# Kernel optimization log

Measured on AMD Instinct MI355X. Metric: run time of the kernel, lower is better.

Reference implementation:

```python
import jax, jax.numpy as jnp
import numpy as np

B, H, S, DK = 4, 16, 2048, 64


def setup_inputs() -> dict:
    key = jax.random.key(0)
    kq, kk, kv, km = jax.random.split(key, 4)
    Q = jax.random.normal(kq, (B, H, S, DK), dtype=jnp.float32)
    K = jax.random.normal(kk, (B, H, S, DK), dtype=jnp.float32)
    V = jax.random.normal(kv, (B, H, S, DK), dtype=jnp.float32)
    mask = (jax.random.uniform(km, (B, 1, S, S)) > 0.1).astype(jnp.float32)
    return {"Q": Q, "K": K, "V": V, "mask": mask}


def reference(Q, K, V, mask):
    d_k = Q.shape[-1]
    # unnormalized exp scores (no max subtraction), multiplicative mask
    scores = jnp.exp(jnp.einsum("bhqd,bhkd->bhqk", Q, K) / jnp.sqrt(jnp.float32(d_k)))
    scores = scores * mask
    attn = scores / (jnp.sum(scores, axis=-1, keepdims=True) + 1e-8)
    return jnp.einsum("bhqk,bhkd->bhqd", attn, V)
```

## Files before the change

kernel.cpp:

```cpp
#include <hip/hip_runtime.h>

namespace {
constexpr int S  = 2048;
constexpr int D  = 64;
constexpr int BQ = 256;
constexpr int BK = 64;
constexpr int NT = 512;
constexpr int NKT = S / BK;

typedef short bf16x8 __attribute__((ext_vector_type(8)));
typedef float f32x4  __attribute__((ext_vector_type(4)));

__device__ inline unsigned short bf16c(float x) {
  __bf16 h = (__bf16)x;
  return __builtin_bit_cast(unsigned short, h);
}
__device__ inline unsigned pk2(float a, float b) {
  return (unsigned)bf16c(a) | ((unsigned)bf16c(b) << 16);
}
__device__ inline void gld_lds16(const void* g, void* l) {
  __builtin_amdgcn_global_load_lds(
      (const __attribute__((address_space(1))) unsigned int*)g,
      (__attribute__((address_space(3))) unsigned int*)l, 16, 0, 0);
}
#if __has_builtin(__builtin_amdgcn_exp2f)
__device__ inline float exp2v(float x) { return __builtin_amdgcn_exp2f(x); }
#else
__device__ inline float exp2v(float x) { return __expf(x * 0.6931471805599453f); }
#endif

__device__ inline int kswz_of_row(int row) {
  return ((row >> 3) & 3) | ((row & 1) << 2);
}

__device__ inline bf16x8 mk_pa(f32x4 s0, f32x4 s1, unsigned mw0, unsigned mw1) {
  float p0 = exp2v(s0[0]) * (float)(mw0 & 0xffu);
  float p1 = exp2v(s0[1]) * (float)((mw0 >> 8) & 0xffu);
  float p2 = exp2v(s0[2]) * (float)((mw0 >> 16) & 0xffu);
  float p3 = exp2v(s0[3]) * (float)(mw0 >> 24);
  float p4 = exp2v(s1[0]) * (float)(mw1 & 0xffu);
  float p5 = exp2v(s1[1]) * (float)((mw1 >> 8) & 0xffu);
  float p6 = exp2v(s1[2]) * (float)((mw1 >> 16) & 0xffu);
  float p7 = exp2v(s1[3]) * (float)(mw1 >> 24);
  uint4 u = make_uint4(pk2(p0, p1), pk2(p2, p3), pk2(p4, p5), pk2(p6, p7));
  return __builtin_bit_cast(bf16x8, u);
}

__global__ __launch_bounds__(256) void prep_k(const float* __restrict__ K,
                                              unsigned short* __restrict__ Kws) {
  int gid = blockIdx.x * 256 + threadIdx.x;
  int row = gid >> 3;
  int g   = gid & 7;
  const float* src = K + (size_t)row * 64 + g * 8;
  float4 a = *(const float4*)src;
  float4 b = *(const float4*)(src + 4);
  uint4 w;
  w.x = pk2(a.x, a.y); w.y = pk2(a.z, a.w);
  w.z = pk2(b.x, b.y); w.w = pk2(b.z, b.w);
  *(uint4*)(Kws + (size_t)row * 64 + ((g ^ kswz_of_row(row)) * 8)) = w;
}

__global__ __launch_bounds__(256) void prep_v(const float* __restrict__ V,
                                              unsigned short* __restrict__ Vws) {
  __shared__ float tl[64 * 68];
  const int t = threadIdx.x;
  const size_t tile = blockIdx.x;
  const float* src = V + tile * (64 * 64);
#pragma unroll
  for (int rep = 0; rep < 4; ++rep) {
    int idx = t + rep * 256;
    int row = idx >> 4, d4 = idx & 15;
    float4 v = *(const float4*)(src + row * 64 + d4 * 4);
    *(float4*)(tl + row * 68 + d4 * 4) = v;
  }
  __syncthreads();
  unsigned short* dstT = Vws + tile * (64 * 64);
#pragma unroll
  for (int rep = 0; rep < 2; ++rep) {
    int d  = (t & 31) + rep * 32;
    int kg = t >> 5;
    float x[8];
#pragma unroll
    for (int j = 0; j < 8; ++j) x[j] = tl[(kg * 8 + j) * 68 + d];
    uint4 w;
    w.x = pk2(x[0], x[1]); w.y = pk2(x[2], x[3]);
    w.z = pk2(x[4], x[5]); w.w = pk2(x[6], x[7]);
    *(uint4*)(dstT + d * 64 + ((kg ^ (d & 7)) * 8)) = w;
  }
}

__global__ __launch_bounds__(256) void prep_m(const float* __restrict__ M,
                                              unsigned char* __restrict__ M2) {
  size_t gid = (size_t)blockIdx.x * 256 + threadIdx.x;
  int g    = (int)(gid & 1);
  int lane = (int)((gid >> 1) & 63);
  int qg   = (int)((gid >> 7) & 63);
  int kt   = (int)((gid >> 13) & 31);
  int b    = (int)(gid >> 18);
  int n16  = lane & 15;
  int quad = (lane >> 4) & 3;
  int q = qg * 32 + g * 16 + n16;
  const float* src = M + ((size_t)b * S + q) * S + kt * 64 + quad * 8;
  unsigned wds[4];
#pragma unroll
  for (int w = 0; w < 4; ++w) {
    int ks = w >> 1, h = w & 1;
    float4 v = *(const float4*)(src + ks * 32 + h * 4);
    unsigned m = 0;
    if (v.x != 0.0f) m |= 0x00000001u;
    if (v.y != 0.0f) m |= 0x00000100u;
    if (v.z != 0.0f) m |= 0x00010000u;
    if (v.w != 0.0f) m |= 0x01000000u;
    wds[w] = m;
  }
  *(uint4*)(M2 + gid * 16) = make_uint4(wds[0], wds[1], wds[2], wds[3]);
}

__global__ __launch_bounds__(NT, 4)
void attn3(const float* __restrict__ Qg, const unsigned char* __restrict__ M2,
           const unsigned short* __restrict__ Kws,
           const unsigned short* __restrict__ Vws,
           float* __restrict__ Og) {
  __shared__ __align__(16) unsigned short sK[2][BK * D];
  __shared__ __align__(16) unsigned short sV[2][BK * D];

  const int t    = threadIdx.x;
  const int wave = t >> 6;
  const int lane = t & 63;
  const int quad = lane >> 4;
  const int n16  = lane & 15;

  const int bh = blockIdx.y;
  const int b  = bh >> 4;
  const int q0 = blockIdx.x * BQ;
  const int qg = blockIdx.x * 8 + wave;

  const unsigned short* Kb = Kws + (size_t)bh * S * D;
  const unsigned short* Vb = Vws + (size_t)bh * S * D;
  const unsigned char* Mp = M2 + (((size_t)b * NKT * 64 + qg) * 64 + lane) * 32;
  constexpr size_t MKT = (size_t)64 * 64 * 32;

  const int h2 = n16 >> 2, rr = n16 & 3;
  const int kswz  = h2 | ((rr & 1) << 2);
  const int koffA = (quad ^ kswz) * 8;
  const int koffB = ((quad + 4) ^ kswz) * 8;
  const int krow0 = (8 * h2 + rr) * 64;

  const int sw = n16 & 7;
  const int ga = (quad ^ sw) * 8;
  const int gb = ((quad + 4) ^ sw) * 8;

  constexpr float QS = 0.18033688011112042f;
  const float* QbA = Qg + ((size_t)bh * S + q0 + wave * 32 + n16) * D;
  bf16x8 aqA[2], aqB[2];
#pragma unroll
  for (int ks = 0; ks < 2; ++ks) {
    const float* qp = QbA + ks * 32 + quad * 8;
    float4 x = *(const float4*)qp;
    float4 y = *(const float4*)(qp + 4);
    bf16x8 a;
    a[0] = (short)bf16c(x.x * QS); a[1] = (short)bf16c(x.y * QS);
    a[2] = (short)bf16c(x.z * QS); a[3] = (short)bf16c(x.w * QS);
    a[4] = (short)bf16c(y.x * QS); a[5] = (short)bf16c(y.y * QS);
    a[6] = (short)bf16c(y.z * QS); a[7] = (short)bf16c(y.w * QS);
    aqA[ks] = a;
    const float* qp2 = qp + 16 * D;
    float4 x2 = *(const float4*)qp2;
    float4 y2 = *(const float4*)(qp2 + 4);
    bf16x8 a2;
    a2[0] = (short)bf16c(x2.x * QS); a2[1] = (short)bf16c(x2.y * QS);
    a2[2] = (short)bf16c(x2.z * QS); a2[3] = (short)bf16c(x2.w * QS);
    a2[4] = (short)bf16c(y2.x * QS); a2[5] = (short)bf16c(y2.y * QS);
    a2[6] = (short)bf16c(y2.z * QS); a2[7] = (short)bf16c(y2.w * QS);
    aqB[ks] = a2;
  }

  bf16x8 ones;
#pragma unroll
  for (int i = 0; i < 8; ++i) ones[i] = (short)0x3F80;

  f32x4 oA[4], oB[4];
#pragma unroll
  for (int nt = 0; nt < 4; ++nt) {
    oA[nt] = (f32x4){0.f, 0.f, 0.f, 0.f};
    oB[nt] = (f32x4){0.f, 0.f, 0.f, 0.f};
  }
  f32x4 rsA = (f32x4){0.f, 0.f, 0.f, 0.f};
  f32x4 rsB = (f32x4){0.f, 0.f, 0.f, 0.f};

  gld_lds16(Kb + wave * 512 + lane * 8, &sK[0][wave * 512]);
  gld_lds16(Vb + wave * 512 + lane * 8, &sV[0][wave * 512]);

#pragma unroll 2
  for (int kt = 0; kt < NKT; ++kt) {
    const int cur = kt & 1, nxt = cur ^ 1;
    __syncthreads();

    uint4 mkA = *(const uint4*)(Mp + (size_t)kt * MKT);
    uint4 mkB = *(const uint4*)(Mp + (size_t)kt * MKT + 16);

    if (kt + 1 < NKT) {
      gld_lds16(Kb + (size_t)(kt + 1) * (BK * D) + wave * 512 + lane * 8,
                &sK[nxt][wave * 512]);
      gld_lds16(Vb + (size_t)(kt + 1) * (BK * D) + wave * 512 + lane * 8,
                &sV[nxt][wave * 512]);
    }

    bf16x8 paA[2], paB[2];
#pragma unroll
    for (int ks = 0; ks < 2; ++ks) {
      const unsigned short* base = &sK[cur][krow0 + ks * 2048];
      bf16x8 k0a = *(const bf16x8*)(base + koffA);
      bf16x8 k0b = *(const bf16x8*)(base + koffB);
      bf16x8 k1a = *(const bf16x8*)(base + 256 + koffA);
      bf16x8 k1b = *(const bf16x8*)(base + 256 + koffB);
      const f32x4 z = (f32x4){0.f, 0.f, 0.f, 0.f};

      f32x4 sA0 = __builtin_amdgcn_mfma_f32_16x16x32_bf16(k0a, aqA[0], z, 0, 0, 0);
      sA0 = __builtin_amdgcn_mfma_f32_16x16x32_bf16(k0b, aqA[1], sA0, 0, 0, 0);
      f32x4 sA1 = __builtin_amdgcn_mfma_f32_16x16x32_bf16(k1a, aqA[0], z, 0, 0, 0);
      sA1 = __builtin_amdgcn_mfma_f32_16x16x32_bf16(k1b, aqA[1], sA1, 0, 0, 0);
      paA[ks] = mk_pa(sA0, sA1, ks ? mkA.z : mkA.x, ks ? mkA.w : mkA.y);

      f32x4 sB0 = __builtin_amdgcn_mfma_f32_16x16x32_bf16(k0a, aqB[0], z, 0, 0, 0);
      sB0 = __builtin_amdgcn_mfma_f32_16x16x32_bf16(k0b, aqB[1], sB0, 0, 0, 0);
      f32x4 sB1 = __builtin_amdgcn_mfma_f32_16x16x32_bf16(k1a, aqB[0], z, 0, 0, 0);
      sB1 = __builtin_amdgcn_mfma_f32_16x16x32_bf16(k1b, aqB[1], sB1, 0, 0, 0);
      paB[ks] = mk_pa(sB0, sB1, ks ? mkB.z : mkB.x, ks ? mkB.w : mkB.y);
    }

    rsA = __builtin_amdgcn_mfma_f32_16x16x32_bf16(ones, paA[0], rsA, 0, 0, 0);
    rsA = __builtin_amdgcn_mfma_f32_16x16x32_bf16(ones, paA[1], rsA, 0, 0, 0);
    rsB = __builtin_amdgcn_mfma_f32_16x16x32_bf16(ones, paB[0], rsB, 0, 0, 0);
    rsB = __builtin_amdgcn_mfma_f32_16x16x32_bf16(ones, paB[1], rsB, 0, 0, 0);

#pragma unroll
    for (int nt = 0; nt < 4; ++nt) {
      const int row = nt * 16 + n16;
      bf16x8 v0 = *(const bf16x8*)(sV[cur] + row * 64 + ga);
      bf16x8 v1 = *(const bf16x8*)(sV[cur] + row * 64 + gb);
      oA[nt] = __builtin_amdgcn_mfma_f32_16x16x32_bf16(v0, paA[0], oA[nt], 0, 0, 0);
      oA[nt] = __builtin_amdgcn_mfma_f32_16x16x32_bf16(v1, paA[1], oA[nt], 0, 0, 0);
      oB[nt] = __builtin_amdgcn_mfma_f32_16x16x32_bf16(v0, paB[0], oB[nt], 0, 0, 0);
      oB[nt] = __builtin_amdgcn_mfma_f32_16x16x32_bf16(v1, paB[1], oB[nt], 0, 0, 0);
    }
  }

  const float invA = 1.0f / (rsA[0] + 1e-8f);
  const float invB = 1.0f / (rsB[0] + 1e-8f);
  float* OA = Og + ((size_t)bh * S + q0 + wave * 32 + n16) * D;
#pragma unroll
  for (int nt = 0; nt < 4; ++nt) {
    float4 wa = make_float4(oA[nt][0] * invA, oA[nt][1] * invA,
                            oA[nt][2] * invA, oA[nt][3] * invA);
    *(float4*)(OA + nt * 16 + quad * 4) = wa;
    float4 wb = make_float4(oB[nt][0] * invB, oB[nt][1] * invB,
                            oB[nt][2] * invB, oB[nt][3] * invB);
    *(float4*)(OA + 16 * D + nt * 16 + quad * 4) = wb;
  }
}
}

extern "C" void kernel_launch(void* const* d_in, const int* in_sizes, int n_in,
                              void* d_out, int out_size, void* d_ws, size_t ws_size,
                              hipStream_t stream) {
  const float* Q = (const float*)d_in[0];
  const float* K = (const float*)d_in[1];
  const float* V = (const float*)d_in[2];
  const float* M = (const float*)d_in[3];
  float* O = (float*)d_out;

  unsigned short* Kws = (unsigned short*)d_ws;
  unsigned short* Vws = Kws + (size_t)64 * S * D;
  unsigned char*  M2  = (unsigned char*)(Vws + (size_t)64 * S * D);

  prep_k<<<dim3(64 * S * D / 8 / 256), 256, 0, stream>>>(K, Kws);
  prep_v<<<dim3(64 * NKT), 256, 0, stream>>>(V, Vws);
  prep_m<<<dim3(4 * NKT * 64 * 64 * 2 / 256), 256, 0, stream>>>(M, M2);
  attn3<<<dim3(S / BQ, 64), NT, 0, stream>>>(Q, M2, Kws, Vws, O);
}
```

Before: 270.7 us.

## Restructure mask prep for coalesced row reads via LDS and change K swizzle

```diff
diff --git a/kernel.cpp b/kernel.cpp
--- a/kernel.cpp
+++ b/kernel.cpp
@@ -30,7 +30,7 @@
 #endif
 
 __device__ inline int kswz_of_row(int row) {
-  return ((row >> 3) & 3) | ((row & 1) << 2);
+  return (row & 3) | (((row >> 3) & 1) << 2);
 }
 
 __device__ inline bf16x8 mk_pa(f32x4 s0, f32x4 s1, unsigned mw0, unsigned mw1) {
@@ -89,31 +89,55 @@
   }
 }
 
-__global__ __launch_bounds__(256) void prep_m(const float* __restrict__ M,
+__global__ __launch_bounds__(512) void prep_m(const float* __restrict__ M,
                                               unsigned char* __restrict__ M2) {
-  size_t gid = (size_t)blockIdx.x * 256 + threadIdx.x;
-  int g    = (int)(gid & 1);
-  int lane = (int)((gid >> 1) & 63);
-  int qg   = (int)((gid >> 7) & 63);
-  int kt   = (int)((gid >> 13) & 31);
-  int b    = (int)(gid >> 18);
-  int n16  = lane & 15;
-  int quad = (lane >> 4) & 3;
-  int q = qg * 32 + g * 16 + n16;
-  const float* src = M + ((size_t)b * S + q) * S + kt * 64 + quad * 8;
-  unsigned wds[4];
-#pragma unroll
-  for (int w = 0; w < 4; ++w) {
-    int ks = w >> 1, h = w & 1;
-    float4 v = *(const float4*)(src + ks * 32 + h * 4);
-    unsigned m = 0;
-    if (v.x != 0.0f) m |= 0x00000001u;
-    if (v.y != 0.0f) m |= 0x00000100u;
-    if (v.z != 0.0f) m |= 0x00010000u;
-    if (v.w != 0.0f) m |= 0x01000000u;
-    wds[w] = m;
-  }
-  *(uint4*)(M2 + gid * 16) = make_uint4(wds[0], wds[1], wds[2], wds[3]);
+  __shared__ unsigned nibs[32][129];
+  const int t  = threadIdx.x;
+  const int b  = blockIdx.x >> 6;
+  const int qg = blockIdx.x & 63;
+  const float* src = M + ((size_t)b * S + (size_t)qg * 32) * S;
+
+#pragma unroll
+  for (int pass = 0; pass < 8; ++pass) {
+    int idx = pass * 512 + t;
+    int q  = idx >> 7;
+    int kc = idx & 127;
+    const float* p = src + (size_t)q * S + kc * 16;
+    unsigned w = 0;
+#pragma unroll
+    for (int j = 0; j < 4; ++j) {
+      float4 v = *(const float4*)(p + j * 4);
+      unsigned nib = (v.x != 0.f ? 1u : 0u) | (v.y != 0.f ? 2u : 0u) |
+                     (v.z != 0.f ? 4u : 0u) | (v.w != 0.f ? 8u : 0u);
+      w |= nib << (8 * j);
+    }
+    nibs[q][kc] = w;
+  }
+  __syncthreads();
+
+  const int e    = t & 127;
+  const int lane = e >> 1, g = e & 1;
+  const int n16  = lane & 15, quad = lane >> 4;
+  const int qq   = g * 16 + n16;
+  const int c    = quad >> 1;
+  const int sh0  = 8 * ((2 * quad) & 3);
+  unsigned char* dstb = M2 + ((size_t)b * NKT * 64 + qg) * 2048 + (size_t)e * 16;
+#pragma unroll
+  for (int i = 0; i < 8; ++i) {
+    int kt = (t >> 7) + i * 4;
+    unsigned d0 = nibs[qq][kt * 4 + c];
+    unsigned d1 = nibs[qq][kt * 4 + 2 + c];
+    unsigned n00 = (d0 >> sh0) & 0xFu;
+    unsigned n01 = (d0 >> (sh0 + 8)) & 0xFu;
+    unsigned n10 = (d1 >> sh0) & 0xFu;
+    unsigned n11 = (d1 >> (sh0 + 8)) & 0xFu;
+    uint4 out;
+    out.x = (n00 * 0x00204081u) & 0x01010101u;
+    out.y = (n01 * 0x00204081u) & 0x01010101u;
+    out.z = (n10 * 0x00204081u) & 0x01010101u;
+    out.w = (n11 * 0x00204081u) & 0x01010101u;
+    *(uint4*)(dstb + (size_t)kt * (64 * 64 * 32)) = out;
+  }
 }
 
 __global__ __launch_bounds__(NT, 4)
@@ -141,9 +165,6 @@
   constexpr size_t MKT = (size_t)64 * 64 * 32;
 
   const int h2 = n16 >> 2, rr = n16 & 3;
-  const int kswz  = h2 | ((rr & 1) << 2);
-  const int koffA = (quad ^ kswz) * 8;
-  const int koffB = ((quad + 4) ^ kswz) * 8;
   const int krow0 = (8 * h2 + rr) * 64;
 
   const int sw = n16 & 7;
@@ -210,10 +231,10 @@
 #pragma unroll
     for (int ks = 0; ks < 2; ++ks) {
       const unsigned short* base = &sK[cur][krow0 + ks * 2048];
-      bf16x8 k0a = *(const bf16x8*)(base + koffA);
-      bf16x8 k0b = *(const bf16x8*)(base + koffB);
-      bf16x8 k1a = *(const bf16x8*)(base + 256 + koffA);
-      bf16x8 k1b = *(const bf16x8*)(base + 256 + koffB);
+      bf16x8 k0a = *(const bf16x8*)(base + ga);
+      bf16x8 k0b = *(const bf16x8*)(base + gb);
+      bf16x8 k1a = *(const bf16x8*)(base + 256 + ga);
+      bf16x8 k1b = *(const bf16x8*)(base + 256 + gb);
       const f32x4 z = (f32x4){0.f, 0.f, 0.f, 0.f};
 
       f32x4 sA0 = __builtin_amdgcn_mfma_f32_16x16x32_bf16(k0a, aqA[0], z, 0, 0, 0);
@@ -276,6 +297,6 @@
 
   prep_k<<<dim3(64 * S * D / 8 / 256), 256, 0, stream>>>(K, Kws);
   prep_v<<<dim3(64 * NKT), 256, 0, stream>>>(V, Vws);
-  prep_m<<<dim3(4 * NKT * 64 * 64 * 2 / 256), 256, 0, stream>>>(M, M2);
+  prep_m<<<dim3(4 * 64), 512, 0, stream>>>(M, M2);
   attn3<<<dim3(S / BQ, 64), NT, 0, stream>>>(Q, M2, Kws, Vws, O);
 }
```

Result: no change. 270.3 us (-0.1%).
